# Kernel optimization log

Hardware: AMD Instinct MI355X
Metric: run time of the kernel (lower is better)

The kernel has to match this reference:

```python
import jax, jax.numpy as jnp
import numpy as np
from jax import lax

B, L, EMB, C, H, NTF = 512, 1024, 4, 64, 64, 200
D2 = 2 * H  # 128, bi-LSTM feature dim


def setup_inputs() -> dict:
    key = jax.random.key(0)
    ks = iter(jax.random.split(key, 48))
    r = lambda shape, s=0.05: jax.random.normal(next(ks), shape, jnp.float32) * s
    inp = {"DNA_x": jax.random.normal(next(ks), (B, L, EMB), jnp.float32)}
    # conv stack: channels 4 -> 64 -> 64, kernel 8
    inp["conv0_w"] = r((C, EMB, 8)); inp["conv0_b"] = r((C,))
    inp["bn0_g"] = 1.0 + r((C,)); inp["bn0_b"] = r((C,))
    inp["bn0_m"] = r((C,)); inp["bn0_v"] = jax.random.uniform(next(ks), (C,), jnp.float32, 0.5, 1.5)
    inp["conv1_w"] = r((C, C, 8)); inp["conv1_b"] = r((C,))
    inp["bn1_g"] = 1.0 + r((C,)); inp["bn1_b"] = r((C,))
    inp["bn1_m"] = r((C,)); inp["bn1_v"] = jax.random.uniform(next(ks), (C,), jnp.float32, 0.5, 1.5)
    # bidirectional LSTM, torch gate order (i, f, g, o)
    for d in ("f", "b"):
        inp[f"wih_{d}"] = r((4 * H, C)); inp[f"whh_{d}"] = r((4 * H, H))
        inp[f"bih_{d}"] = r((4 * H,)); inp[f"bhh_{d}"] = r((4 * H,))
    # Bahdanau attention: W1, W2: 128->128, V: 128->NTF
    inp["W1_w"] = r((D2, D2)); inp["W1_b"] = r((D2,))
    inp["W2_w"] = r((D2, D2)); inp["W2_b"] = r((D2,))
    inp["V_w"] = r((NTF, D2)); inp["V_b"] = r((NTF,))
    # per-TF heads stacked: Linear(128->64), Linear(64->1)
    inp["fc1_w"] = r((NTF, 64, D2)); inp["fc1_b"] = r((NTF, 64))
    inp["fc2_w"] = r((NTF, 64)); inp["fc2_b"] = r((NTF,))
    return inp


def _conv(x, w, b):  # x:[B,Cin,L], w:[Cout,Cin,K]
    y = lax.conv_general_dilated(x, w, (1,), "VALID",
                                 dimension_numbers=("NCH", "OIH", "NCH"))
    return y + b[:, None]


def _bn(x, g, b, m, v):  # eval-mode BatchNorm1d over channel dim
    return (x - m[:, None]) * (g[:, None] / jnp.sqrt(v[:, None] + 1e-5)) + b[:, None]


def _lstm(x, Wih, Whh, bih, bhh):  # x:[B,T,D] -> ([B,T,H], h_T:[B,H])
    Bn = x.shape[0]
    Hh = Whh.shape[1]
    bias = bih + bhh
    def step(carry, xt):
        h, c = carry
        g = xt @ Wih.T + h @ Whh.T + bias
        i, f, gg, o = jnp.split(g, 4, axis=-1)
        c = jax.nn.sigmoid(f) * c + jax.nn.sigmoid(i) * jnp.tanh(gg)
        h = jax.nn.sigmoid(o) * jnp.tanh(c)
        return (h, c), h
    init = (jnp.zeros((Bn, Hh), x.dtype), jnp.zeros((Bn, Hh), x.dtype))
    (hT, _), hs = lax.scan(step, init, jnp.swapaxes(x, 0, 1))
    return jnp.swapaxes(hs, 0, 1), hT


def reference(DNA_x, conv0_w, conv0_b, bn0_g, bn0_b, bn0_m, bn0_v,
              conv1_w, conv1_b, bn1_g, bn1_b, bn1_m, bn1_v,
              wih_f, whh_f, bih_f, bhh_f, wih_b, whh_b, bih_b, bhh_b,
              W1_w, W1_b, W2_w, W2_b, V_w, V_b,
              fc1_w, fc1_b, fc2_w, fc2_b):
    x = jnp.swapaxes(DNA_x, 1, 2)                      # [B,EMB,L]
    x = jax.nn.relu(_bn(_conv(x, conv0_w, conv0_b), bn0_g, bn0_b, bn0_m, bn0_v))
    x = lax.reduce_window(x, -jnp.inf, lax.max, (1, 1, 4), (1, 1, 4), "VALID")
    x = jax.nn.relu(_bn(_conv(x, conv1_w, conv1_b), bn1_g, bn1_b, bn1_m, bn1_v))
    x = jnp.swapaxes(x, 1, 2)                          # [B,T,C], T=247
    hf, hTf = _lstm(x, wih_f, whh_f, bih_f, bhh_f)
    hb, hTb = _lstm(x[:, ::-1, :], wih_b, whh_b, bih_b, bhh_b)
    values = jnp.concatenate([hf, hb[:, ::-1, :]], axis=-1)   # [B,T,2H]
    # torch h_n.view(B, 2H) on [2,B,H]: flat reshape (replicated exactly)
    h_n = jnp.stack([hTf, hTb], axis=0).reshape(values.shape[0], -1)
    # Bahdanau attention with NTF query heads
    score = jnp.tanh(values @ W1_w.T + W1_b + (h_n @ W2_w.T + W2_b)[:, None, :]) @ V_w.T + V_b
    aw = jax.nn.softmax(score, axis=1)                 # [B,T,NTF], softmax over time
    context = jnp.einsum("btd,btk->bkd", values, aw)   # [B,NTF,2H]
    # fused per-TF MLP heads: grouped GEMM over NTF
    h1 = jax.nn.relu(jnp.einsum("bkd,kod->bko", context, fc1_w) + fc1_b)
    out = jnp.einsum("bko,ko->bk", h1, fc2_w) + fc2_b  # [B,NTF]
    return out
```

## Files before the change

kernel.cpp:

```cpp
#include <hip/hip_runtime.h>
#include <math.h>

#define BB 512
#define LL 1024
#define EMB 4
#define CC 64
#define NTF 200
#define TT 247
#define LP 254
#define D2 128

typedef __attribute__((ext_vector_type(8))) short short8;
typedef __attribute__((ext_vector_type(4))) float f32x4;
typedef __attribute__((ext_vector_type(4))) unsigned int uint4v;

__device__ __forceinline__ float sigf(float x) {
  return __builtin_amdgcn_rcpf(1.0f + __expf(-x));
}
__device__ __forceinline__ float tanhff(float x) {
  return 1.0f - 2.0f * __builtin_amdgcn_rcpf(__expf(2.0f * x) + 1.0f);
}

__device__ __forceinline__ void lds_barrier() {
  __builtin_amdgcn_s_waitcnt(0xC07F);
  __builtin_amdgcn_s_barrier();
}

__device__ __forceinline__ unsigned short bfr(float f) {
  unsigned u = __builtin_bit_cast(unsigned, f);
  u += 0x7fffu + ((u >> 16) & 1u);
  return (unsigned short)(u >> 16);
}

__global__ __launch_bounds__(256) void k_cvt(const float* __restrict__ w0,
    const float* __restrict__ w1,
    const float* __restrict__ wihf, const float* __restrict__ whhf,
    const float* __restrict__ wihb, const float* __restrict__ whhb,
    const float* __restrict__ bihf, const float* __restrict__ bhhf,
    const float* __restrict__ bihb, const float* __restrict__ bhhb,
    const float* __restrict__ W1w, const float* __restrict__ Vw,
    const float* __restrict__ f1w,
    unsigned short* __restrict__ wbf0, unsigned short* __restrict__ wbf1r,
    unsigned short* __restrict__ wihbf, unsigned short* __restrict__ whhbf,
    float* __restrict__ lbias,
    unsigned short* __restrict__ W1bf, unsigned short* __restrict__ Vbf,
    unsigned short* __restrict__ f1bf)
{
  int i = blockIdx.x * 256 + threadIdx.x;
  if (i < 2048) wbf0[i] = bfr(w0[i]);
  if (i < 32768) {
    int co = i >> 9, k = (i >> 6) & 7, ci = i & 63;
    wbf1r[i] = bfr(w1[co * 512 + ci * 8 + k]);
  }
  if (i < 16384) {
    wihbf[i] = bfr(wihf[i]);
    wihbf[16384 + i] = bfr(wihb[i]);
    whhbf[i] = bfr(whhf[i]);
    whhbf[16384 + i] = bfr(whhb[i]);
    W1bf[i] = bfr(W1w[i]);
  }
  if (i < 26624) {
    int row = i >> 7;
    Vbf[i] = (row < NTF) ? bfr(Vw[i]) : (unsigned short)0;
  }
  if (i < 256) {
    lbias[i] = bihf[i] + bhhf[i];
    lbias[256 + i] = bihb[i] + bhhb[i];
  }
  if (i < 1638400) f1bf[i] = bfr(f1w[i]);
}

__global__ __launch_bounds__(256) void k_conv0m(const float* __restrict__ x,
    const unsigned short* __restrict__ wbf0,
    const float* __restrict__ b0, const float* __restrict__ g0,
    const float* __restrict__ be0, const float* __restrict__ m0,
    const float* __restrict__ v0, unsigned short* __restrict__ pbf)
{
  int b = blockIdx.x, l0 = blockIdx.y * 64;
  __shared__ float xs[71 * 4];
  __shared__ float sc[64], sb[64];
  int tid = threadIdx.x;
  for (int j = tid; j < 71; j += 256) {
    int l = l0 + j;
    float4 xv = (l < LL) ? *(const float4*)(x + ((size_t)b * LL + l) * EMB)
                         : make_float4(0.f, 0.f, 0.f, 0.f);
    *(float4*)(xs + j * 4) = xv;
  }
  if (tid < 64) {
    float s = g0[tid] * rsqrtf(v0[tid] + 1e-5f);
    sc[tid] = s;
    sb[tid] = (b0[tid] - m0[tid]) * s + be0[tid];
  }
  __syncthreads();
  int w = tid >> 6, lane = tid & 63, nl = lane & 15, quad = lane >> 4;
  const float* ap = xs + (w * 16 + nl) * 4 + quad;
  short8 af;
  #pragma unroll
  for (int j = 0; j < 8; ++j) af[j] = (short)bfr(ap[j * 4]);
  f32x4 acc[4];
  #pragma unroll
  for (int nt = 0; nt < 4; ++nt) {
    short8 bf = __builtin_bit_cast(short8,
        *(const uint4v*)(wbf0 + ((nt * 16 + nl) * 32 + quad * 8)));
    acc[nt] = (f32x4){0.f, 0.f, 0.f, 0.f};
    acc[nt] = __builtin_amdgcn_mfma_f32_16x16x32_bf16(af, bf, acc[nt], 0, 0, 0);
  }
  int t = (l0 >> 2) + w * 4 + quad;
  if (t < LP) {
    #pragma unroll
    for (int nt = 0; nt < 4; ++nt) {
      int c = nt * 16 + nl;
      float scc = sc[c], sbc = sb[c];
      float mx = -1e30f;
      #pragma unroll
      for (int r = 0; r < 4; ++r) mx = fmaxf(mx, acc[nt][r] * scc + sbc);
      pbf[((size_t)b * LP + t) * CC + c] = bfr(fmaxf(mx, 0.0f));
    }
  }
}

__global__ __launch_bounds__(256) void k_conv1m(const unsigned short* __restrict__ pbf,
    const unsigned short* __restrict__ wbf1r,
    const float* __restrict__ b1, const float* __restrict__ g1,
    const float* __restrict__ be1, const float* __restrict__ m1,
    const float* __restrict__ v1, unsigned short* __restrict__ x2bf)
{
  int b = blockIdx.x, t0 = blockIdx.y * 64;
  __shared__ __align__(16) unsigned short ps[71 * 72];
  __shared__ float sc[64], sb[64];
  int tid = threadIdx.x;
  for (int j = tid; j < 71 * 32; j += 256) {
    int tl = j >> 5, cu = j & 31;
    int t = t0 + tl;
    unsigned v = (t < LP) ? *(const unsigned*)(pbf + ((size_t)b * LP + t) * CC + cu * 2) : 0u;
    *(unsigned*)(&ps[tl * 72 + cu * 2]) = v;
  }
  if (tid < 64) {
    float s = g1[tid] * rsqrtf(v1[tid] + 1e-5f);
    sc[tid] = s;
    sb[tid] = (b1[tid] - m1[tid]) * s + be1[tid];
  }
  __syncthreads();
  int w = tid >> 6, lane = tid & 63, nl = lane & 15, quad = lane >> 4;
  int tlb = w * 16 + nl;
  f32x4 acc[4];
  #pragma unroll
  for (int nt = 0; nt < 4; ++nt) acc[nt] = (f32x4){0.f, 0.f, 0.f, 0.f};
  #pragma unroll
  for (int k8 = 0; k8 < 8; ++k8) {
    short8 af0 = __builtin_bit_cast(short8,
        *(const uint4v*)(&ps[(tlb + k8) * 72 + 0 + quad * 8]));
    short8 af1 = __builtin_bit_cast(short8,
        *(const uint4v*)(&ps[(tlb + k8) * 72 + 32 + quad * 8]));
    #pragma unroll
    for (int nt = 0; nt < 4; ++nt) {
      int co = nt * 16 + nl;
      short8 bf0 = __builtin_bit_cast(short8,
          *(const uint4v*)(wbf1r + (size_t)co * 512 + k8 * 64 + 0 + quad * 8));
      short8 bf1 = __builtin_bit_cast(short8,
          *(const uint4v*)(wbf1r + (size_t)co * 512 + k8 * 64 + 32 + quad * 8));
      acc[nt] = __builtin_amdgcn_mfma_f32_16x16x32_bf16(af0, bf0, acc[nt], 0, 0, 0);
      acc[nt] = __builtin_amdgcn_mfma_f32_16x16x32_bf16(af1, bf1, acc[nt], 0, 0, 0);
    }
  }
  #pragma unroll
  for (int nt = 0; nt < 4; ++nt) {
    int c = nt * 16 + nl;
    float scc = sc[c], sbc = sb[c];
    #pragma unroll
    for (int r = 0; r < 4; ++r) {
      int t = t0 + w * 16 + quad * 4 + r;
      if (t < TT)
        x2bf[((size_t)b * TT + t) * CC + c] = bfr(fmaxf(acc[nt][r] * scc + sbc, 0.0f));
    }
  }
}

__global__ __launch_bounds__(256) void k_lstm_m(const unsigned short* __restrict__ x2bf,
    const unsigned short* __restrict__ wihbf, const unsigned short* __restrict__ whhbf,
    const float* __restrict__ lbias,
    unsigned short* __restrict__ values, float* __restrict__ hT)
{
  int b0 = blockIdx.x * 16;
  int dir = blockIdx.y;
  int tid = threadIdx.x;
  int w = tid >> 6, lane = tid & 63, l15 = lane & 15, quad = lane >> 4;
  int h0 = w * 16;
  const unsigned short* wih = wihbf + dir * 16384;
  const unsigned short* whh = whhbf + dir * 16384;

  short8 bx[4][2], bh[4][2];
  float bias_v[4];
  #pragma unroll
  for (int g = 0; g < 4; ++g) {
    int row = g * 64 + h0 + l15;
    #pragma unroll
    for (int k = 0; k < 2; ++k) {
      bx[g][k] = __builtin_bit_cast(short8, *(const uint4v*)(wih + row * 64 + k * 32 + quad * 8));
      bh[g][k] = __builtin_bit_cast(short8, *(const uint4v*)(whh + row * 64 + k * 32 + quad * 8));
    }
    bias_v[g] = lbias[dir * 256 + g * 64 + h0 + l15];
  }

  __shared__ __align__(16) unsigned short xls[2][8][16 * 72];
  __shared__ __align__(16) unsigned short hist[8][16 * 72];
  for (int j = tid; j < 16 * 72; j += 256) hist[7][j] = 0;

  int bl = tid >> 4, d4 = tid & 15;
  const unsigned short* xrow = x2bf + ((size_t)(b0 + bl) * TT) * 64 + d4 * 4;

  uint2 xr[8];
  #pragma unroll
  for (int k = 0; k < 8; ++k) {
    int t = dir ? (TT - 1 - k) : k;
    xr[k] = *(const uint2*)(xrow + (size_t)t * 64);
  }
  #pragma unroll
  for (int k = 0; k < 8; ++k)
    *(uint2*)(&xls[0][k][bl * 72 + d4 * 4]) = xr[k];
  #pragma unroll
  for (int k = 0; k < 8; ++k) {
    int s = 8 + k;
    int t = dir ? (TT - 1 - s) : s;
    xr[k] = *(const uint2*)(xrow + (size_t)t * 64);
  }
  __syncthreads();

  float cst[4] = {0.f, 0.f, 0.f, 0.f};
  for (int c = 0; c < 31; ++c) {
    int buf = c & 1;
    #pragma unroll
    for (int sl = 0; sl < 8; ++sl) {
      int hp = (sl + 7) & 7;
      short8 ax0 = __builtin_bit_cast(short8, *(const uint4v*)(&xls[buf][sl][l15 * 72 + quad * 8]));
      short8 ax1 = __builtin_bit_cast(short8, *(const uint4v*)(&xls[buf][sl][l15 * 72 + 32 + quad * 8]));
      short8 ah0 = __builtin_bit_cast(short8, *(const uint4v*)(&hist[hp][l15 * 72 + quad * 8]));
      short8 ah1 = __builtin_bit_cast(short8, *(const uint4v*)(&hist[hp][l15 * 72 + 32 + quad * 8]));
      f32x4 aX[4], aH[4];
      #pragma unroll
      for (int g = 0; g < 4; ++g) {
        aX[g] = (f32x4){bias_v[g], bias_v[g], bias_v[g], bias_v[g]};
        aX[g] = __builtin_amdgcn_mfma_f32_16x16x32_bf16(ax0, bx[g][0], aX[g], 0, 0, 0);
        aX[g] = __builtin_amdgcn_mfma_f32_16x16x32_bf16(ax1, bx[g][1], aX[g], 0, 0, 0);
        aH[g] = (f32x4){0.f, 0.f, 0.f, 0.f};
        aH[g] = __builtin_amdgcn_mfma_f32_16x16x32_bf16(ah0, bh[g][0], aH[g], 0, 0, 0);
        aH[g] = __builtin_amdgcn_mfma_f32_16x16x32_bf16(ah1, bh[g][1], aH[g], 0, 0, 0);
      }
      #pragma unroll
      for (int r = 0; r < 4; ++r) {
        float ig = sigf(aX[0][r] + aH[0][r]);
        float fg = sigf(aX[1][r] + aH[1][r]);
        float gg = tanhff(aX[2][r] + aH[2][r]);
        float og = sigf(aX[3][r] + aH[3][r]);
        cst[r] = fg * cst[r] + ig * gg;
        float hh = og * tanhff(cst[r]);
        hist[sl][(quad * 4 + r) * 72 + h0 + l15] = bfr(hh);
        if (c == 30 && sl == 6) {
          int bglob = b0 + quad * 4 + r;
          hT[((size_t)dir * BB + bglob) * 64 + h0 + l15] = hh;
        }
      }
      lds_barrier();
    }
    uint4v dv[4];
    #pragma unroll
    for (int i = 0; i < 4; ++i) {
      int flat = i * 256 + tid;
      int sl = flat >> 7, wb = (flat >> 3) & 15, c8 = flat & 7;
      dv[i] = *(const uint4v*)(&hist[sl][wb * 72 + c8 * 8]);
    }
    #pragma unroll
    for (int i = 0; i < 4; ++i) {
      int flat = i * 256 + tid;
      int sl = flat >> 7, wb = (flat >> 3) & 15, c8 = flat & 7;
      int s = c * 8 + sl;
      if (s < TT) {
        int t = dir ? (TT - 1 - s) : s;
        *(uint4v*)(values + ((size_t)(b0 + wb) * TT + t) * D2 + dir * 64 + c8 * 8) = dv[i];
      }
    }
    if (c < 30) {
      #pragma unroll
      for (int k = 0; k < 8; ++k)
        *(uint2*)(&xls[1 - buf][k][bl * 72 + d4 * 4]) = xr[k];
      #pragma unroll
      for (int k = 0; k < 8; ++k) {
        int s2 = (c + 2) * 8 + k;
        if (s2 > TT - 1) s2 = TT - 1;
        int t2 = dir ? (TT - 1 - s2) : s2;
        xr[k] = *(const uint2*)(xrow + (size_t)t2 * 64);
      }
    }
    lds_barrier();
  }
}

__global__ __launch_bounds__(128) void k_q2(const float* __restrict__ hT,
    const float* __restrict__ W2, const float* __restrict__ W2b,
    float* __restrict__ q2)
{
  int b = blockIdx.x;
  int tid = threadIdx.x;
  __shared__ float4 hn4[32];
  ((float*)hn4)[tid] = hT[(size_t)b * 128 + tid];
  __syncthreads();
  const float4* w4 = (const float4*)(W2 + (size_t)tid * 128);
  float a = W2b[tid];
  #pragma unroll
  for (int j = 0; j < 32; ++j) {
    float4 w = w4[j]; float4 h = hn4[j];
    a += w.x * h.x + w.y * h.y + w.z * h.z + w.w * h.w;
  }
  q2[(size_t)b * 128 + tid] = a;
}

__global__ __launch_bounds__(256) void k_score_m(const unsigned short* __restrict__ vbf,
    const unsigned short* __restrict__ W1bf, const float* __restrict__ W1b,
    const float* __restrict__ q2, const unsigned short* __restrict__ Vbf,
    const float* __restrict__ Vb, unsigned short* __restrict__ scoreT)
{
  int b = blockIdx.x, t0 = blockIdx.y * 64;
  int tid = threadIdx.x, w = tid >> 6, lane = tid & 63, l15 = lane & 15, quad = lane >> 4;
  __shared__ unsigned short us[64 * 136];
  __shared__ unsigned short sc2[64 * 213];
  const unsigned short* arow = vbf + ((size_t)b * TT + t0 + w * 16 + l15) * 128;
  short8 ax[4];
  #pragma unroll
  for (int ks = 0; ks < 4; ++ks)
    ax[ks] = __builtin_bit_cast(short8, *(const uint4v*)(arow + ks * 32 + quad * 8));
  #pragma unroll
  for (int nt = 0; nt < 8; ++nt) {
    int n = nt * 16 + l15;
    float base = W1b[n] + q2[(size_t)b * 128 + n];
    f32x4 acc = (f32x4){base, base, base, base};
    #pragma unroll
    for (int ks = 0; ks < 4; ++ks) {
      short8 bf = __builtin_bit_cast(short8,
          *(const uint4v*)(W1bf + (size_t)n * 128 + ks * 32 + quad * 8));
      acc = __builtin_amdgcn_mfma_f32_16x16x32_bf16(ax[ks], bf, acc, 0, 0, 0);
    }
    #pragma unroll
    for (int r = 0; r < 4; ++r)
      us[(w * 16 + quad * 4 + r) * 136 + nt * 16 + l15] = bfr(tanhff(acc[r]));
  }
  __syncthreads();
  short8 au[4];
  #pragma unroll
  for (int ks = 0; ks < 4; ++ks)
    au[ks] = __builtin_bit_cast(short8, *(const uint4v*)(&us[(w * 16 + l15) * 136 + ks * 32 + quad * 8]));
  for (int nt2 = 0; nt2 < 13; ++nt2) {
    int n = nt2 * 16 + l15;
    float b2 = (n < NTF) ? Vb[n] : 0.0f;
    f32x4 a2 = (f32x4){b2, b2, b2, b2};
    #pragma unroll
    for (int ks = 0; ks < 4; ++ks) {
      short8 bf = __builtin_bit_cast(short8,
          *(const uint4v*)(Vbf + (size_t)n * 128 + ks * 32 + quad * 8));
      a2 = __builtin_amdgcn_mfma_f32_16x16x32_bf16(au[ks], bf, a2, 0, 0, 0);
    }
    #pragma unroll
    for (int r = 0; r < 4; ++r) {
      int tl = w * 16 + quad * 4 + r;
      sc2[tl * 213 + n] = bfr(a2[r]);
    }
  }
  __syncthreads();
  int tg = tid & 3;
  #pragma unroll
  for (int pp = 0; pp < 4; ++pp) {
    int nrow = pp * 64 + (tid >> 2);
    if (nrow < NTF) {
      unsigned uu[8];
      #pragma unroll
      for (int k2 = 0; k2 < 8; ++k2) {
        unsigned lo = sc2[(tg * 16 + k2 * 2) * 213 + nrow];
        unsigned hi = sc2[(tg * 16 + k2 * 2 + 1) * 213 + nrow];
        uu[k2] = lo | (hi << 16);
      }
      size_t dst = ((size_t)b * 208 + nrow) * 256 + t0 + tg * 16;
      *(uint4v*)(scoreT + dst) = (uint4v){uu[0], uu[1], uu[2], uu[3]};
      *(uint4v*)(scoreT + dst + 8) = (uint4v){uu[4], uu[5], uu[6], uu[7]};
    }
  }
}

__global__ __launch_bounds__(256) void k_softmax(unsigned short* __restrict__ scoreT,
    float* __restrict__ sinv)
{
  int b = blockIdx.x, nc = blockIdx.y;
  int tid = threadIdx.x;
  int n = nc * 64 + (tid >> 2), tg = tid & 3;
  if (n >= NTF) return;
  unsigned short* row = scoreT + ((size_t)b * 208 + n) * 256 + tg * 64;
  uint4v ld[8];
  #pragma unroll
  for (int i = 0; i < 8; ++i) ld[i] = *(const uint4v*)(row + i * 8);
  float m = -1e30f;
  #pragma unroll
  for (int i = 0; i < 8; ++i) {
    #pragma unroll
    for (int u = 0; u < 4; ++u) {
      unsigned xv = ld[i][u];
      int t0 = tg * 64 + i * 8 + u * 2;
      float a = __builtin_bit_cast(float, xv << 16);
      float c = __builtin_bit_cast(float, xv & 0xffff0000u);
      if (t0 < TT) m = fmaxf(m, a);
      if (t0 + 1 < TT) m = fmaxf(m, c);
    }
  }
  m = fmaxf(m, __shfl_xor(m, 1, 64));
  m = fmaxf(m, __shfl_xor(m, 2, 64));
  float s = 0.0f;
  #pragma unroll
  for (int i = 0; i < 8; ++i) {
    uint4v ov;
    #pragma unroll
    for (int u = 0; u < 4; ++u) {
      unsigned xv = ld[i][u];
      int t0 = tg * 64 + i * 8 + u * 2;
      float a = __builtin_bit_cast(float, xv << 16);
      float c = __builtin_bit_cast(float, xv & 0xffff0000u);
      float ea = (t0 < TT) ? __expf(a - m) : 0.0f;
      float ec = (t0 + 1 < TT) ? __expf(c - m) : 0.0f;
      s += ea + ec;
      ov[u] = (unsigned)bfr(ea) | ((unsigned)bfr(ec) << 16);
    }
    *(uint4v*)(row + i * 8) = ov;
  }
  s += __shfl_xor(s, 1, 64);
  s += __shfl_xor(s, 2, 64);
  if (tg == 0) sinv[(size_t)b * NTF + n] = __builtin_amdgcn_rcpf(s);
}

__global__ __launch_bounds__(256) void k_ctx_m(const unsigned short* __restrict__ vbf,
    const unsigned short* __restrict__ scoreT, const float* __restrict__ sinv,
    unsigned short* __restrict__ ctxbf)
{
  int b = blockIdx.x;
  int tid = threadIdx.x, w = tid >> 6, lane = tid & 63, l15 = lane & 15, quad = lane >> 4;
  __shared__ __align__(16) unsigned short vt[128 * 264];
  __shared__ float sls[208];
  for (int flat = tid; flat < 247 * 64; flat += 256) {
    int t = flat >> 6, dp = flat & 63;
    unsigned v = *(const unsigned*)(vbf + ((size_t)b * TT + t) * D2 + dp * 2);
    vt[(dp * 2) * 264 + t] = (unsigned short)(v & 0xffffu);
    vt[(dp * 2 + 1) * 264 + t] = (unsigned short)(v >> 16);
  }
  for (int j = tid; j < 128 * 9; j += 256) {
    int d = j / 9, t = 247 + (j % 9);
    vt[d * 264 + t] = 0;
  }
  for (int j = tid; j < 208; j += 256) sls[j] = (j < NTF) ? sinv[(size_t)b * NTF + j] : 0.0f;
  __syncthreads();

  const unsigned short* abase = scoreT + (size_t)b * 208 * 256;
  for (int mi = 0; mi < 4; ++mi) {
    int mt = w + 4 * mi;
    if (mt >= 13) continue;
    const unsigned short* arow = abase + (size_t)(mt * 16 + l15) * 256;
    short8 af[8];
    #pragma unroll
    for (int ks = 0; ks < 8; ++ks)
      af[ks] = __builtin_bit_cast(short8, *(const uint4v*)(arow + ks * 32 + quad * 8));
    f32x4 acc[8];
    #pragma unroll
    for (int dt = 0; dt < 8; ++dt) {
      acc[dt] = (f32x4){0.f, 0.f, 0.f, 0.f};
      #pragma unroll
      for (int ks = 0; ks < 8; ++ks) {
        short8 bf = __builtin_bit_cast(short8,
            *(const uint4v*)(&vt[(dt * 16 + l15) * 264 + ks * 32 + quad * 8]));
        acc[dt] = __builtin_amdgcn_mfma_f32_16x16x32_bf16(af[ks], bf, acc[dt], 0, 0, 0);
      }
    }
    #pragma unroll
    for (int r = 0; r < 4; ++r) {
      int n = mt * 16 + quad * 4 + r;
      if (n < NTF) {
        float rs = sls[n];
        #pragma unroll
        for (int dt = 0; dt < 8; ++dt)
          ctxbf[((size_t)b * NTF + n) * D2 + dt * 16 + l15] = bfr(acc[dt][r] * rs);
      }
    }
  }
}

__global__ __launch_bounds__(256) void k_heads_m(const unsigned short* __restrict__ ctxbf,
    const unsigned short* __restrict__ f1bf, const float* __restrict__ fc1b,
    const float* __restrict__ fc2w, const float* __restrict__ fc2b,
    float* __restrict__ out)
{
  int n = blockIdx.x;
  int b0 = blockIdx.y * 128;
  int tid = threadIdx.x, w = tid >> 6, lane = tid & 63, l15 = lane & 15, quad = lane >> 4;
  short8 bfr_[4][4];
  float f1bv[4], f2v[4];
  #pragma unroll
  for (int nt = 0; nt < 4; ++nt) {
    int o = nt * 16 + l15;
    #pragma unroll
    for (int ks = 0; ks < 4; ++ks)
      bfr_[nt][ks] = __builtin_bit_cast(short8,
          *(const uint4v*)(f1bf + ((size_t)n * 64 + o) * 128 + ks * 32 + quad * 8));
    f1bv[nt] = fc1b[n * 64 + o];
    f2v[nt] = fc2w[n * 64 + o];
  }
  float f2b = fc2b[n];
  #pragma unroll
  for (int mi = 0; mi < 2; ++mi) {
    int m16 = (w * 2 + mi) * 16;
    const unsigned short* arow = ctxbf + ((size_t)(b0 + m16 + l15) * NTF + n) * 128;
    short8 af[4];
    #pragma unroll
    for (int ks = 0; ks < 4; ++ks)
      af[ks] = __builtin_bit_cast(short8, *(const uint4v*)(arow + ks * 32 + quad * 8));
    f32x4 acc[4];
    #pragma unroll
    for (int nt = 0; nt < 4; ++nt) {
      acc[nt] = (f32x4){0.f, 0.f, 0.f, 0.f};
      #pragma unroll
      for (int ks = 0; ks < 4; ++ks)
        acc[nt] = __builtin_amdgcn_mfma_f32_16x16x32_bf16(af[ks], bfr_[nt][ks], acc[nt], 0, 0, 0);
    }
    #pragma unroll
    for (int r = 0; r < 4; ++r) {
      float part = 0.0f;
      #pragma unroll
      for (int nt = 0; nt < 4; ++nt)
        part += fmaxf(acc[nt][r] + f1bv[nt], 0.0f) * f2v[nt];
      part += __shfl_xor(part, 1, 64);
      part += __shfl_xor(part, 2, 64);
      part += __shfl_xor(part, 4, 64);
      part += __shfl_xor(part, 8, 64);
      if (l15 == 0) {
        int bb = b0 + m16 + quad * 4 + r;
        out[(size_t)bb * NTF + n] = part + f2b;
      }
    }
  }
}

extern "C" void kernel_launch(void* const* d_in, const int* in_sizes, int n_in,
                              void* d_out, int out_size, void* d_ws, size_t ws_size,
                              hipStream_t stream)
{
  const float* x    = (const float*)d_in[0];
  const float* c0w  = (const float*)d_in[1];
  const float* c0b  = (const float*)d_in[2];
  const float* g0   = (const float*)d_in[3];
  const float* be0  = (const float*)d_in[4];
  const float* m0   = (const float*)d_in[5];
  const float* v0   = (const float*)d_in[6];
  const float* c1w  = (const float*)d_in[7];
  const float* c1b  = (const float*)d_in[8];
  const float* g1   = (const float*)d_in[9];
  const float* be1  = (const float*)d_in[10];
  const float* m1   = (const float*)d_in[11];
  const float* v1   = (const float*)d_in[12];
  const float* wihf = (const float*)d_in[13];
  const float* whhf = (const float*)d_in[14];
  const float* bihf = (const float*)d_in[15];
  const float* bhhf = (const float*)d_in[16];
  const float* wihb = (const float*)d_in[17];
  const float* whhb = (const float*)d_in[18];
  const float* bihb = (const float*)d_in[19];
  const float* bhhb = (const float*)d_in[20];
  const float* W1w  = (const float*)d_in[21];
  const float* W1b  = (const float*)d_in[22];
  const float* W2w  = (const float*)d_in[23];
  const float* W2b  = (const float*)d_in[24];
  const float* Vw   = (const float*)d_in[25];
  const float* Vb   = (const float*)d_in[26];
  const float* f1w  = (const float*)d_in[27];
  const float* f1b  = (const float*)d_in[28];
  const float* f2w  = (const float*)d_in[29];
  const float* f2b  = (const float*)d_in[30];

  float* ws = (float*)d_ws;
  unsigned short* scoreT = (unsigned short*)ws;
  unsigned short* pbf  = (unsigned short*)ws;
  unsigned short* x2bf = (unsigned short*)(ws + 8323072);
  unsigned short* vbf  = (unsigned short*)(ws + 25292800);
  float* hT     = ws + 33387520;
  float* q2     = ws + 33453056;
  float* sinv   = ws + 33518592;
  unsigned short* ctxbf = (unsigned short*)(ws + 33620992);
  unsigned short* wbf0  = (unsigned short*)(ws + 46728192);
  unsigned short* wbf1r = (unsigned short*)(ws + 46729216);
  unsigned short* wihbf = (unsigned short*)(ws + 46745600);
  unsigned short* whhbf = (unsigned short*)(ws + 46761984);
  float* lbias          = ws + 46778368;
  unsigned short* W1bf  = (unsigned short*)(ws + 46778880);
  unsigned short* Vbf   = (unsigned short*)(ws + 46787072);
  unsigned short* f1bf  = (unsigned short*)(ws + 46800384);
  float* out    = (float*)d_out;

  k_cvt<<<dim3(6400), 256, 0, stream>>>(c0w, c1w, wihf, whhf, wihb, whhb,
                                        bihf, bhhf, bihb, bhhb, W1w, Vw, f1w,
                                        wbf0, wbf1r, wihbf, whhbf, lbias, W1bf, Vbf, f1bf);
  k_conv0m<<<dim3(BB, 16), 256, 0, stream>>>(x, wbf0, c0b, g0, be0, m0, v0, pbf);
  k_conv1m<<<dim3(BB, 4), 256, 0, stream>>>(pbf, wbf1r, c1b, g1, be1, m1, v1, x2bf);
  k_lstm_m<<<dim3(BB / 16, 2), 256, 0, stream>>>(x2bf, wihbf, whhbf, lbias, vbf, hT);
  k_q2<<<dim3(BB), 128, 0, stream>>>(hT, W2w, W2b, q2);
  k_score_m<<<dim3(BB, 4), 256, 0, stream>>>(vbf, W1bf, W1b, q2, Vbf, Vb, scoreT);
  k_softmax<<<dim3(BB, 4), 256, 0, stream>>>(scoreT, sinv);
  k_ctx_m<<<dim3(BB), 256, 0, stream>>>(vbf, scoreT, sinv, ctxbf);
  k_heads_m<<<dim3(NTF, 4), 256, 0, stream>>>(ctxbf, f1bf, f1b, f2w, f2b, out);
}
```

Before: 523.3 us.

## Interleave two batch tiles per LSTM block and fold log2e into gate weights

The LSTM kernel now processes two independent 16-row batch tiles per block, so MFMA and transcendental work from one tile can hide the latency of the other's recurrence. The grid is halved to 32x2 blocks. Input rows are loaded straight into registers one step ahead, replacing the LDS staging buffer. Gate weights and biases are pre-scaled by log2(e) (2·log2(e) for the g gate) so activations can use exp2 directly. The trade-off is half as many blocks (64) on a GPU with many CUs, plus extra register pressure and a little extra bf16 rounding error from the pre-scaled weights.

```diff
diff --git a/kernel.cpp b/kernel.cpp
--- a/kernel.cpp
+++ b/kernel.cpp
@@ -14,11 +14,32 @@
 typedef __attribute__((ext_vector_type(4))) float f32x4;
 typedef __attribute__((ext_vector_type(4))) unsigned int uint4v;
 
+#define L2E  1.4426950408889634f
+#define TL2E 2.8853900817779268f
+
 __device__ __forceinline__ float sigf(float x) {
   return __builtin_amdgcn_rcpf(1.0f + __expf(-x));
 }
 __device__ __forceinline__ float tanhff(float x) {
   return 1.0f - 2.0f * __builtin_amdgcn_rcpf(__expf(2.0f * x) + 1.0f);
+}
+
+__device__ __forceinline__ float ex2(float x) {
+#if defined(__has_builtin)
+#if __has_builtin(__builtin_amdgcn_exp2f)
+  return __builtin_amdgcn_exp2f(x);
+#else
+  return exp2f(x);
+#endif
+#else
+  return exp2f(x);
+#endif
+}
+__device__ __forceinline__ float sig2(float y) {
+  return __builtin_amdgcn_rcpf(1.0f + ex2(-y));
+}
+__device__ __forceinline__ float tanh2(float y) {
+  return 1.0f - 2.0f * __builtin_amdgcn_rcpf(ex2(y) + 1.0f);
 }
 
 __device__ __forceinline__ void lds_barrier() {
@@ -53,10 +74,11 @@
     wbf1r[i] = bfr(w1[co * 512 + ci * 8 + k]);
   }
   if (i < 16384) {
-    wihbf[i] = bfr(wihf[i]);
-    wihbf[16384 + i] = bfr(wihb[i]);
-    whhbf[i] = bfr(whhf[i]);
-    whhbf[16384 + i] = bfr(whhb[i]);
+    float s = ((i >> 12) == 2) ? TL2E : L2E;
+    wihbf[i] = bfr(wihf[i] * s);
+    wihbf[16384 + i] = bfr(wihb[i] * s);
+    whhbf[i] = bfr(whhf[i] * s);
+    whhbf[16384 + i] = bfr(whhb[i] * s);
     W1bf[i] = bfr(W1w[i]);
   }
   if (i < 26624) {
@@ -64,8 +86,9 @@
     Vbf[i] = (row < NTF) ? bfr(Vw[i]) : (unsigned short)0;
   }
   if (i < 256) {
-    lbias[i] = bihf[i] + bhhf[i];
-    lbias[256 + i] = bihb[i] + bhhb[i];
+    float s = ((i >> 6) == 2) ? TL2E : L2E;
+    lbias[i] = (bihf[i] + bhhf[i]) * s;
+    lbias[256 + i] = (bihb[i] + bhhb[i]) * s;
   }
   if (i < 1638400) f1bf[i] = bfr(f1w[i]);
 }
@@ -181,8 +204,8 @@
     const float* __restrict__ lbias,
     unsigned short* __restrict__ values, float* __restrict__ hT)
 {
-  int b0 = blockIdx.x * 16;
   int dir = blockIdx.y;
+  int b0A = blockIdx.x * 32, b0B = b0A + 16;
   int tid = threadIdx.x;
   int w = tid >> 6, lane = tid & 63, l15 = lane & 15, quad = lane >> 4;
   int h0 = w * 16;
@@ -202,93 +225,102 @@
     bias_v[g] = lbias[dir * 256 + g * 64 + h0 + l15];
   }
 
-  __shared__ __align__(16) unsigned short xls[2][8][16 * 72];
-  __shared__ __align__(16) unsigned short hist[8][16 * 72];
-  for (int j = tid; j < 16 * 72; j += 256) hist[7][j] = 0;
-
-  int bl = tid >> 4, d4 = tid & 15;
-  const unsigned short* xrow = x2bf + ((size_t)(b0 + bl) * TT) * 64 + d4 * 4;
-
-  uint2 xr[8];
-  #pragma unroll
-  for (int k = 0; k < 8; ++k) {
-    int t = dir ? (TT - 1 - k) : k;
-    xr[k] = *(const uint2*)(xrow + (size_t)t * 64);
-  }
-  #pragma unroll
-  for (int k = 0; k < 8; ++k)
-    *(uint2*)(&xls[0][k][bl * 72 + d4 * 4]) = xr[k];
-  #pragma unroll
-  for (int k = 0; k < 8; ++k) {
-    int s = 8 + k;
-    int t = dir ? (TT - 1 - s) : s;
-    xr[k] = *(const uint2*)(xrow + (size_t)t * 64);
-  }
+  __shared__ __align__(16) unsigned short histA[8][16 * 72];
+  __shared__ __align__(16) unsigned short histB[8][16 * 72];
+  for (int j = tid; j < 16 * 72; j += 256) { histA[7][j] = 0; histB[7][j] = 0; }
   __syncthreads();
 
-  float cst[4] = {0.f, 0.f, 0.f, 0.f};
+  const unsigned short* xA = x2bf + ((size_t)(b0A + l15) * TT) * 64 + quad * 8;
+  const unsigned short* xB = x2bf + ((size_t)(b0B + l15) * TT) * 64 + quad * 8;
+
+  uint4v xra[2][2], xrb[2][2];
+  {
+    size_t o0 = (size_t)(dir ? (TT - 1) : 0) * 64;
+    xra[0][0] = *(const uint4v*)(xA + o0);
+    xra[0][1] = *(const uint4v*)(xA + o0 + 32);
+    xrb[0][0] = *(const uint4v*)(xB + o0);
+    xrb[0][1] = *(const uint4v*)(xB + o0 + 32);
+  }
+
+  float cA[4] = {0.f, 0.f, 0.f, 0.f}, cB[4] = {0.f, 0.f, 0.f, 0.f};
+
   for (int c = 0; c < 31; ++c) {
-    int buf = c & 1;
     #pragma unroll
     for (int sl = 0; sl < 8; ++sl) {
-      int hp = (sl + 7) & 7;
-      short8 ax0 = __builtin_bit_cast(short8, *(const uint4v*)(&xls[buf][sl][l15 * 72 + quad * 8]));
-      short8 ax1 = __builtin_bit_cast(short8, *(const uint4v*)(&xls[buf][sl][l15 * 72 + 32 + quad * 8]));
-      short8 ah0 = __builtin_bit_cast(short8, *(const uint4v*)(&hist[hp][l15 * 72 + quad * 8]));
-      short8 ah1 = __builtin_bit_cast(short8, *(const uint4v*)(&hist[hp][l15 * 72 + 32 + quad * 8]));
-      f32x4 aX[4], aH[4];
-      #pragma unroll
-      for (int g = 0; g < 4; ++g) {
-        aX[g] = (f32x4){bias_v[g], bias_v[g], bias_v[g], bias_v[g]};
-        aX[g] = __builtin_amdgcn_mfma_f32_16x16x32_bf16(ax0, bx[g][0], aX[g], 0, 0, 0);
-        aX[g] = __builtin_amdgcn_mfma_f32_16x16x32_bf16(ax1, bx[g][1], aX[g], 0, 0, 0);
-        aH[g] = (f32x4){0.f, 0.f, 0.f, 0.f};
-        aH[g] = __builtin_amdgcn_mfma_f32_16x16x32_bf16(ah0, bh[g][0], aH[g], 0, 0, 0);
-        aH[g] = __builtin_amdgcn_mfma_f32_16x16x32_bf16(ah1, bh[g][1], aH[g], 0, 0, 0);
-      }
-      #pragma unroll
-      for (int r = 0; r < 4; ++r) {
-        float ig = sigf(aX[0][r] + aH[0][r]);
-        float fg = sigf(aX[1][r] + aH[1][r]);
-        float gg = tanhff(aX[2][r] + aH[2][r]);
-        float og = sigf(aX[3][r] + aH[3][r]);
-        cst[r] = fg * cst[r] + ig * gg;
-        float hh = og * tanhff(cst[r]);
-        hist[sl][(quad * 4 + r) * 72 + h0 + l15] = bfr(hh);
-        if (c == 30 && sl == 6) {
-          int bglob = b0 + quad * 4 + r;
-          hT[((size_t)dir * BB + bglob) * 64 + h0 + l15] = hh;
+      int s = c * 8 + sl;
+      const int par = sl & 1;
+      if (s < TT) {
+        int hp = (sl + 7) & 7;
+        short8 ahA0 = __builtin_bit_cast(short8, *(const uint4v*)(&histA[hp][l15 * 72 + quad * 8]));
+        short8 ahA1 = __builtin_bit_cast(short8, *(const uint4v*)(&histA[hp][l15 * 72 + 32 + quad * 8]));
+        short8 ahB0 = __builtin_bit_cast(short8, *(const uint4v*)(&histB[hp][l15 * 72 + quad * 8]));
+        short8 ahB1 = __builtin_bit_cast(short8, *(const uint4v*)(&histB[hp][l15 * 72 + 32 + quad * 8]));
+        short8 axA0 = __builtin_bit_cast(short8, xra[par][0]);
+        short8 axA1 = __builtin_bit_cast(short8, xra[par][1]);
+        short8 axB0 = __builtin_bit_cast(short8, xrb[par][0]);
+        short8 axB1 = __builtin_bit_cast(short8, xrb[par][1]);
+        {
+          int sn = s + 1; if (sn > TT - 1) sn = TT - 1;
+          size_t on = (size_t)(dir ? (TT - 1 - sn) : sn) * 64;
+          xra[par ^ 1][0] = *(const uint4v*)(xA + on);
+          xra[par ^ 1][1] = *(const uint4v*)(xA + on + 32);
+          xrb[par ^ 1][0] = *(const uint4v*)(xB + on);
+          xrb[par ^ 1][1] = *(const uint4v*)(xB + on + 32);
+        }
+        f32x4 aA[4], aB[4];
+        #pragma unroll
+        for (int g = 0; g < 4; ++g) {
+          aA[g] = (f32x4){bias_v[g], bias_v[g], bias_v[g], bias_v[g]};
+          aA[g] = __builtin_amdgcn_mfma_f32_16x16x32_bf16(axA0, bx[g][0], aA[g], 0, 0, 0);
+          aA[g] = __builtin_amdgcn_mfma_f32_16x16x32_bf16(axA1, bx[g][1], aA[g], 0, 0, 0);
+          aA[g] = __builtin_amdgcn_mfma_f32_16x16x32_bf16(ahA0, bh[g][0], aA[g], 0, 0, 0);
+          aA[g] = __builtin_amdgcn_mfma_f32_16x16x32_bf16(ahA1, bh[g][1], aA[g], 0, 0, 0);
+          aB[g] = (f32x4){bias_v[g], bias_v[g], bias_v[g], bias_v[g]};
+          aB[g] = __builtin_amdgcn_mfma_f32_16x16x32_bf16(axB0, bx[g][0], aB[g], 0, 0, 0);
+          aB[g] = __builtin_amdgcn_mfma_f32_16x16x32_bf16(axB1, bx[g][1], aB[g], 0, 0, 0);
+          aB[g] = __builtin_amdgcn_mfma_f32_16x16x32_bf16(ahB0, bh[g][0], aB[g], 0, 0, 0);
+          aB[g] = __builtin_amdgcn_mfma_f32_16x16x32_bf16(ahB1, bh[g][1], aB[g], 0, 0, 0);
+        }
+        #pragma unroll
+        for (int r = 0; r < 4; ++r) {
+          int hw = (quad * 4 + r) * 72 + h0 + l15;
+          {
+            float ig = sig2(aA[0][r]);
+            float fg = sig2(aA[1][r]);
+            float gg = tanh2(aA[2][r]);
+            float og = sig2(aA[3][r]);
+            cA[r] = fg * cA[r] + ig * gg;
+            float hh = og * tanh2(cA[r] * TL2E);
+            histA[sl][hw] = bfr(hh);
+            if (s == TT - 1)
+              hT[((size_t)dir * BB + (b0A + quad * 4 + r)) * 64 + h0 + l15] = hh;
+          }
+          {
+            float ig = sig2(aB[0][r]);
+            float fg = sig2(aB[1][r]);
+            float gg = tanh2(aB[2][r]);
+            float og = sig2(aB[3][r]);
+            cB[r] = fg * cB[r] + ig * gg;
+            float hh = og * tanh2(cB[r] * TL2E);
+            histB[sl][hw] = bfr(hh);
+            if (s == TT - 1)
+              hT[((size_t)dir * BB + (b0B + quad * 4 + r)) * 64 + h0 + l15] = hh;
+          }
         }
       }
       lds_barrier();
     }
-    uint4v dv[4];
     #pragma unroll
     for (int i = 0; i < 4; ++i) {
       int flat = i * 256 + tid;
-      int sl = flat >> 7, wb = (flat >> 3) & 15, c8 = flat & 7;
-      dv[i] = *(const uint4v*)(&hist[sl][wb * 72 + c8 * 8]);
-    }
-    #pragma unroll
-    for (int i = 0; i < 4; ++i) {
-      int flat = i * 256 + tid;
-      int sl = flat >> 7, wb = (flat >> 3) & 15, c8 = flat & 7;
-      int s = c * 8 + sl;
+      int sl2 = flat >> 7, wb = (flat >> 3) & 15, c8 = flat & 7;
+      int s = c * 8 + sl2;
       if (s < TT) {
+        uint4v dvA = *(const uint4v*)(&histA[sl2][wb * 72 + c8 * 8]);
+        uint4v dvB = *(const uint4v*)(&histB[sl2][wb * 72 + c8 * 8]);
         int t = dir ? (TT - 1 - s) : s;
-        *(uint4v*)(values + ((size_t)(b0 + wb) * TT + t) * D2 + dir * 64 + c8 * 8) = dv[i];
-      }
-    }
-    if (c < 30) {
-      #pragma unroll
-      for (int k = 0; k < 8; ++k)
-        *(uint2*)(&xls[1 - buf][k][bl * 72 + d4 * 4]) = xr[k];
-      #pragma unroll
-      for (int k = 0; k < 8; ++k) {
-        int s2 = (c + 2) * 8 + k;
-        if (s2 > TT - 1) s2 = TT - 1;
-        int t2 = dir ? (TT - 1 - s2) : s2;
-        xr[k] = *(const uint2*)(xrow + (size_t)t2 * 64);
+        *(uint4v*)(values + ((size_t)(b0A + wb) * TT + t) * D2 + dir * 64 + c8 * 8) = dvA;
+        *(uint4v*)(values + ((size_t)(b0B + wb) * TT + t) * D2 + dir * 64 + c8 * 8) = dvB;
       }
     }
     lds_barrier();
@@ -601,7 +633,7 @@
                                         wbf0, wbf1r, wihbf, whhbf, lbias, W1bf, Vbf, f1bf);
   k_conv0m<<<dim3(BB, 16), 256, 0, stream>>>(x, wbf0, c0b, g0, be0, m0, v0, pbf);
   k_conv1m<<<dim3(BB, 4), 256, 0, stream>>>(pbf, wbf1r, c1b, g1, be1, m1, v1, x2bf);
-  k_lstm_m<<<dim3(BB / 16, 2), 256, 0, stream>>>(x2bf, wihbf, whhbf, lbias, vbf, hT);
+  k_lstm_m<<<dim3(BB / 32, 2), 256, 0, stream>>>(x2bf, wihbf, whhbf, lbias, vbf, hT);
   k_q2<<<dim3(BB), 128, 0, stream>>>(hT, W2w, W2b, q2);
   k_score_m<<<dim3(BB, 4), 256, 0, stream>>>(vbf, W1bf, W1b, q2, Vbf, Vb, scoreT);
   k_softmax<<<dim3(BB, 4), 256, 0, stream>>>(scoreT, sinv);
```

New measurement: 598.4 us. 1.14x slower.

## Pipeline LSTM input projection in registers, prescale gates for exp2, transpose ctx layout

Applied to the files above, without the earlier changes.

The LSTM kernel drops the LDS staging of x. Each lane now loads its own x fragment straight from global memory two steps ahead and computes the input-projection MFMA one step early, so it overlaps with the recurrent chain. The LSTM weights and biases are prescaled by log2(e) (twice that for the g gate), so the activations use a raw exp2, and the input and g-gate products share one reciprocal. The steps past TT are now skipped. The context buffer moves to [NTF][B][D2] layout so the heads kernel reads contiguous rows, at the cost of scattered writes in the context kernel and some extra register pressure.

```diff
diff --git a/kernel.cpp b/kernel.cpp
--- a/kernel.cpp
+++ b/kernel.cpp
@@ -14,11 +14,24 @@
 typedef __attribute__((ext_vector_type(4))) float f32x4;
 typedef __attribute__((ext_vector_type(4))) unsigned int uint4v;
 
+#define L2E  1.4426950408889634f
+#define TL2E 2.8853900817779268f
+
 __device__ __forceinline__ float sigf(float x) {
   return __builtin_amdgcn_rcpf(1.0f + __expf(-x));
 }
 __device__ __forceinline__ float tanhff(float x) {
   return 1.0f - 2.0f * __builtin_amdgcn_rcpf(__expf(2.0f * x) + 1.0f);
+}
+
+__device__ __forceinline__ float ex2(float x) {
+  return __builtin_amdgcn_exp2f(x);
+}
+__device__ __forceinline__ float sig2(float y) {
+  return __builtin_amdgcn_rcpf(1.0f + ex2(-y));
+}
+__device__ __forceinline__ float tanh2(float y) {
+  return 1.0f - 2.0f * __builtin_amdgcn_rcpf(ex2(y) + 1.0f);
 }
 
 __device__ __forceinline__ void lds_barrier() {
@@ -53,10 +66,11 @@
     wbf1r[i] = bfr(w1[co * 512 + ci * 8 + k]);
   }
   if (i < 16384) {
-    wihbf[i] = bfr(wihf[i]);
-    wihbf[16384 + i] = bfr(wihb[i]);
-    whhbf[i] = bfr(whhf[i]);
-    whhbf[16384 + i] = bfr(whhb[i]);
+    float s = ((i >> 12) == 2) ? TL2E : L2E;
+    wihbf[i] = bfr(wihf[i] * s);
+    wihbf[16384 + i] = bfr(wihb[i] * s);
+    whhbf[i] = bfr(whhf[i] * s);
+    whhbf[16384 + i] = bfr(whhb[i] * s);
     W1bf[i] = bfr(W1w[i]);
   }
   if (i < 26624) {
@@ -64,8 +78,9 @@
     Vbf[i] = (row < NTF) ? bfr(Vw[i]) : (unsigned short)0;
   }
   if (i < 256) {
-    lbias[i] = bihf[i] + bhhf[i];
-    lbias[256 + i] = bihb[i] + bhhb[i];
+    float s = ((i >> 6) == 2) ? TL2E : L2E;
+    lbias[i] = (bihf[i] + bhhf[i]) * s;
+    lbias[256 + i] = (bihb[i] + bhhb[i]) * s;
   }
   if (i < 1638400) f1bf[i] = bfr(f1w[i]);
 }
@@ -181,8 +196,8 @@
     const float* __restrict__ lbias,
     unsigned short* __restrict__ values, float* __restrict__ hT)
 {
+  int dir = blockIdx.y;
   int b0 = blockIdx.x * 16;
-  int dir = blockIdx.y;
   int tid = threadIdx.x;
   int w = tid >> 6, lane = tid & 63, l15 = lane & 15, quad = lane >> 4;
   int h0 = w * 16;
@@ -202,93 +217,97 @@
     bias_v[g] = lbias[dir * 256 + g * 64 + h0 + l15];
   }
 
-  __shared__ __align__(16) unsigned short xls[2][8][16 * 72];
   __shared__ __align__(16) unsigned short hist[8][16 * 72];
   for (int j = tid; j < 16 * 72; j += 256) hist[7][j] = 0;
-
-  int bl = tid >> 4, d4 = tid & 15;
-  const unsigned short* xrow = x2bf + ((size_t)(b0 + bl) * TT) * 64 + d4 * 4;
-
-  uint2 xr[8];
-  #pragma unroll
-  for (int k = 0; k < 8; ++k) {
-    int t = dir ? (TT - 1 - k) : k;
-    xr[k] = *(const uint2*)(xrow + (size_t)t * 64);
-  }
-  #pragma unroll
-  for (int k = 0; k < 8; ++k)
-    *(uint2*)(&xls[0][k][bl * 72 + d4 * 4]) = xr[k];
-  #pragma unroll
-  for (int k = 0; k < 8; ++k) {
-    int s = 8 + k;
-    int t = dir ? (TT - 1 - s) : s;
-    xr[k] = *(const uint2*)(xrow + (size_t)t * 64);
-  }
   __syncthreads();
 
+  const unsigned short* xp = x2bf + ((size_t)(b0 + l15) * TT) * 64 + quad * 8;
+
+  uint4v xr[2][2];
+  f32x4 aX[2][4];
+  {
+    size_t o0 = (size_t)(dir ? (TT - 1) : 0) * 64;
+    xr[0][0] = *(const uint4v*)(xp + o0);
+    xr[0][1] = *(const uint4v*)(xp + o0 + 32);
+    short8 a0 = __builtin_bit_cast(short8, xr[0][0]);
+    short8 a1 = __builtin_bit_cast(short8, xr[0][1]);
+    #pragma unroll
+    for (int g = 0; g < 4; ++g) {
+      aX[0][g] = (f32x4){bias_v[g], bias_v[g], bias_v[g], bias_v[g]};
+      aX[0][g] = __builtin_amdgcn_mfma_f32_16x16x32_bf16(a0, bx[g][0], aX[0][g], 0, 0, 0);
+      aX[0][g] = __builtin_amdgcn_mfma_f32_16x16x32_bf16(a1, bx[g][1], aX[0][g], 0, 0, 0);
+    }
+    size_t o1 = (size_t)(dir ? (TT - 2) : 1) * 64;
+    xr[1][0] = *(const uint4v*)(xp + o1);
+    xr[1][1] = *(const uint4v*)(xp + o1 + 32);
+  }
+
   float cst[4] = {0.f, 0.f, 0.f, 0.f};
+
   for (int c = 0; c < 31; ++c) {
-    int buf = c & 1;
     #pragma unroll
     for (int sl = 0; sl < 8; ++sl) {
-      int hp = (sl + 7) & 7;
-      short8 ax0 = __builtin_bit_cast(short8, *(const uint4v*)(&xls[buf][sl][l15 * 72 + quad * 8]));
-      short8 ax1 = __builtin_bit_cast(short8, *(const uint4v*)(&xls[buf][sl][l15 * 72 + 32 + quad * 8]));
-      short8 ah0 = __builtin_bit_cast(short8, *(const uint4v*)(&hist[hp][l15 * 72 + quad * 8]));
-      short8 ah1 = __builtin_bit_cast(short8, *(const uint4v*)(&hist[hp][l15 * 72 + 32 + quad * 8]));
-      f32x4 aX[4], aH[4];
-      #pragma unroll
-      for (int g = 0; g < 4; ++g) {
-        aX[g] = (f32x4){bias_v[g], bias_v[g], bias_v[g], bias_v[g]};
-        aX[g] = __builtin_amdgcn_mfma_f32_16x16x32_bf16(ax0, bx[g][0], aX[g], 0, 0, 0);
-        aX[g] = __builtin_amdgcn_mfma_f32_16x16x32_bf16(ax1, bx[g][1], aX[g], 0, 0, 0);
-        aH[g] = (f32x4){0.f, 0.f, 0.f, 0.f};
-        aH[g] = __builtin_amdgcn_mfma_f32_16x16x32_bf16(ah0, bh[g][0], aH[g], 0, 0, 0);
-        aH[g] = __builtin_amdgcn_mfma_f32_16x16x32_bf16(ah1, bh[g][1], aH[g], 0, 0, 0);
-      }
-      #pragma unroll
-      for (int r = 0; r < 4; ++r) {
-        float ig = sigf(aX[0][r] + aH[0][r]);
-        float fg = sigf(aX[1][r] + aH[1][r]);
-        float gg = tanhff(aX[2][r] + aH[2][r]);
-        float og = sigf(aX[3][r] + aH[3][r]);
-        cst[r] = fg * cst[r] + ig * gg;
-        float hh = og * tanhff(cst[r]);
-        hist[sl][(quad * 4 + r) * 72 + h0 + l15] = bfr(hh);
-        if (c == 30 && sl == 6) {
-          int bglob = b0 + quad * 4 + r;
-          hT[((size_t)dir * BB + bglob) * 64 + h0 + l15] = hh;
+      int s = c * 8 + sl;
+      const int par = sl & 1;
+      if (s < TT) {
+        int hp = (sl + 7) & 7;
+        short8 ah0 = __builtin_bit_cast(short8, *(const uint4v*)(&hist[hp][l15 * 72 + quad * 8]));
+        short8 ah1 = __builtin_bit_cast(short8, *(const uint4v*)(&hist[hp][l15 * 72 + 32 + quad * 8]));
+        f32x4 aH[4];
+        #pragma unroll
+        for (int g = 0; g < 4; ++g) {
+          aH[g] = (f32x4){0.f, 0.f, 0.f, 0.f};
+          aH[g] = __builtin_amdgcn_mfma_f32_16x16x32_bf16(ah0, bh[g][0], aH[g], 0, 0, 0);
+          aH[g] = __builtin_amdgcn_mfma_f32_16x16x32_bf16(ah1, bh[g][1], aH[g], 0, 0, 0);
+        }
+        {
+          short8 a0 = __builtin_bit_cast(short8, xr[par ^ 1][0]);
+          short8 a1 = __builtin_bit_cast(short8, xr[par ^ 1][1]);
+          #pragma unroll
+          for (int g = 0; g < 4; ++g) {
+            aX[par ^ 1][g] = (f32x4){bias_v[g], bias_v[g], bias_v[g], bias_v[g]};
+            aX[par ^ 1][g] = __builtin_amdgcn_mfma_f32_16x16x32_bf16(a0, bx[g][0], aX[par ^ 1][g], 0, 0, 0);
+            aX[par ^ 1][g] = __builtin_amdgcn_mfma_f32_16x16x32_bf16(a1, bx[g][1], aX[par ^ 1][g], 0, 0, 0);
+          }
+        }
+        {
+          int sn = s + 2; if (sn > TT - 1) sn = TT - 1;
+          size_t on = (size_t)(dir ? (TT - 1 - sn) : sn) * 64;
+          xr[par][0] = *(const uint4v*)(xp + on);
+          xr[par][1] = *(const uint4v*)(xp + on + 32);
+        }
+        #pragma unroll
+        for (int r = 0; r < 4; ++r) {
+          float yi = aX[par][0][r] + aH[0][r];
+          float yf = aX[par][1][r] + aH[1][r];
+          float yg = aX[par][2][r] + aH[2][r];
+          float yo = aX[par][3][r] + aH[3][r];
+          float Fi = ex2(-yi);
+          float Ff = ex2(-yf);
+          float Eg = ex2(yg);
+          float fg = __builtin_amdgcn_rcpf(1.0f + Ff);
+          float igg = (Eg - 1.0f) * __builtin_amdgcn_rcpf((1.0f + Fi) * (Eg + 1.0f));
+          cst[r] = fg * cst[r] + igg;
+          float og = __builtin_amdgcn_rcpf(1.0f + ex2(-yo));
+          float hh = og * tanh2(cst[r] * TL2E);
+          hist[sl][(quad * 4 + r) * 72 + h0 + l15] = bfr(hh);
+          if (s == TT - 1) {
+            int bglob = b0 + quad * 4 + r;
+            hT[((size_t)dir * BB + bglob) * 64 + h0 + l15] = hh;
+          }
         }
       }
       lds_barrier();
     }
-    uint4v dv[4];
     #pragma unroll
     for (int i = 0; i < 4; ++i) {
       int flat = i * 256 + tid;
-      int sl = flat >> 7, wb = (flat >> 3) & 15, c8 = flat & 7;
-      dv[i] = *(const uint4v*)(&hist[sl][wb * 72 + c8 * 8]);
-    }
-    #pragma unroll
-    for (int i = 0; i < 4; ++i) {
-      int flat = i * 256 + tid;
-      int sl = flat >> 7, wb = (flat >> 3) & 15, c8 = flat & 7;
-      int s = c * 8 + sl;
+      int sl2 = flat >> 7, wb = (flat >> 3) & 15, c8 = flat & 7;
+      int s = c * 8 + sl2;
       if (s < TT) {
+        uint4v dv = *(const uint4v*)(&hist[sl2][wb * 72 + c8 * 8]);
         int t = dir ? (TT - 1 - s) : s;
-        *(uint4v*)(values + ((size_t)(b0 + wb) * TT + t) * D2 + dir * 64 + c8 * 8) = dv[i];
-      }
-    }
-    if (c < 30) {
-      #pragma unroll
-      for (int k = 0; k < 8; ++k)
-        *(uint2*)(&xls[1 - buf][k][bl * 72 + d4 * 4]) = xr[k];
-      #pragma unroll
-      for (int k = 0; k < 8; ++k) {
-        int s2 = (c + 2) * 8 + k;
-        if (s2 > TT - 1) s2 = TT - 1;
-        int t2 = dir ? (TT - 1 - s2) : s2;
-        xr[k] = *(const uint2*)(xrow + (size_t)t2 * 64);
+        *(uint4v*)(values + ((size_t)(b0 + wb) * TT + t) * D2 + dir * 64 + c8 * 8) = dv;
       }
     }
     lds_barrier();
@@ -480,7 +499,7 @@
         float rs = sls[n];
         #pragma unroll
         for (int dt = 0; dt < 8; ++dt)
-          ctxbf[((size_t)b * NTF + n) * D2 + dt * 16 + l15] = bfr(acc[dt][r] * rs);
+          ctxbf[((size_t)n * BB + b) * D2 + dt * 16 + l15] = bfr(acc[dt][r] * rs);
       }
     }
   }
@@ -510,7 +529,7 @@
   #pragma unroll
   for (int mi = 0; mi < 2; ++mi) {
     int m16 = (w * 2 + mi) * 16;
-    const unsigned short* arow = ctxbf + ((size_t)(b0 + m16 + l15) * NTF + n) * 128;
+    const unsigned short* arow = ctxbf + ((size_t)n * BB + (b0 + m16 + l15)) * 128;
     short8 af[4];
     #pragma unroll
     for (int ks = 0; ks < 4; ++ks)
```

Result: no change. 523.7 us (+0.1%).
